# Kernel tuning notes

Hardware: AMD Instinct MI355X
Metric: run time of the kernel (lower is better)

Reference implementation:

```python
import jax, jax.numpy as jnp
import numpy as np

NUM_HEADS = 16


def setup_inputs() -> dict:
    key = jax.random.key(0)
    ks = jax.random.split(key, 6)
    B, S, E = 2, 2048, 1024
    scale = 1.0 / np.sqrt(E)
    return {
        "x": jax.random.normal(ks[0], (B, S, E), dtype=jnp.float32),
        "mask": jnp.ones((B, S), dtype=jnp.int32),
        "Wq": jax.random.normal(ks[1], (E, E), dtype=jnp.float32) * scale,
        "bq": jnp.zeros((E,), dtype=jnp.float32),
        "Wk": jax.random.normal(ks[2], (E, E), dtype=jnp.float32) * scale,
        "bk": jnp.zeros((E,), dtype=jnp.float32),
        "Wv": jax.random.normal(ks[3], (E, E), dtype=jnp.float32) * scale,
        "bv": jnp.zeros((E,), dtype=jnp.float32),
        "Wo": jax.random.normal(ks[4], (E, E), dtype=jnp.float32) * scale,
        "bo": jnp.zeros((E,), dtype=jnp.float32),
    }


def reference(x, mask, Wq, bq, Wk, bk, Wv, bv, Wo, bo):
    B, S, E = x.shape
    H = NUM_HEADS
    D = E // H

    def heads(t):  # [B,S,E] -> [B,H,S,D]
        return t.reshape(B, S, H, D).transpose(0, 2, 1, 3)

    q = heads(x @ Wq + bq)
    k = heads(x @ Wk + bk)
    v = heads(x @ Wv + bv)

    # scaled dot-product scores [B,H,S,S]
    scores = jnp.einsum("bhsd,bhtd->bhst", q, k) / jnp.sqrt(jnp.float32(D))
    m = mask.astype(jnp.float32)[:, None, None, :]  # key-side padding mask
    scores = scores + (-1e9) * (1.0 - m)
    weights = jax.nn.softmax(scores, axis=-1)
    attn = jnp.einsum("bhst,bhtd->bhsd", weights, v)

    concat = attn.transpose(0, 2, 1, 3).reshape(B, S, E)
    return concat @ Wo + bo
```

## Files before the change

kernel.cpp:

```cpp
#include <hip/hip_runtime.h>
#include <stdint.h>

#define E_DIM   1024
#define HNUM    16
#define DH      64
#define BATCH   2
#define SEQ     2048
#define M_TOT   (BATCH*SEQ)
#define LOG2E   1.44269504088896340736f

typedef __bf16 bf16x8 __attribute__((ext_vector_type(8)));
typedef __bf16 bf16x4 __attribute__((ext_vector_type(4)));
typedef float  f32x4  __attribute__((ext_vector_type(4)));
typedef float  f32x16 __attribute__((ext_vector_type(16)));
typedef unsigned short u16;
typedef unsigned int   u32;
typedef unsigned long long u64;
typedef u16 u16x8 __attribute__((ext_vector_type(8)));
typedef u32 u32x2 __attribute__((ext_vector_type(2)));
typedef u32 u32x4 __attribute__((ext_vector_type(4)));

__device__ __forceinline__ u16 f2bf(float f) {
    u32 u = __builtin_bit_cast(u32, f);
    u32 r = 0x7FFFu + ((u >> 16) & 1u);
    return (u16)((u + r) >> 16);
}

__device__ __forceinline__ void gload_lds16(const u16* g, u16* l) {
    __builtin_amdgcn_global_load_lds(
        (const __attribute__((address_space(1))) u32*)g,
        (__attribute__((address_space(3))) u32*)l, 16, 0, 0);
}

__device__ __forceinline__ u32 cvt_pk_bf16(float lo, float hi) {
    u32 r;
    asm("v_cvt_pk_bf16_f32 %0, %1, %2" : "=v"(r) : "v"(lo), "v"(hi));
    return r;
}

#define MFMA16(a,b,c) __builtin_amdgcn_mfma_f32_16x16x32_bf16((a),(b),(c),0,0,0)
#define MFMA32(a,b,c) __builtin_amdgcn_mfma_f32_32x32x16_bf16((a),(b),(c),0,0,0)

__global__ __launch_bounds__(256) void cast_x_kernel(const float* __restrict__ x,
                                                     u16* __restrict__ out, int n) {
    int idx = (blockIdx.x * 256 + threadIdx.x) * 4;
    if (idx < n) {
        float4 v = *reinterpret_cast<const float4*>(x + idx);
        ushort4 o;
        o.x = f2bf(v.x); o.y = f2bf(v.y); o.z = f2bf(v.z); o.w = f2bf(v.w);
        *reinterpret_cast<ushort4*>(out + idx) = o;
    }
}

__global__ __launch_bounds__(256) void maskbits_kernel(const int* __restrict__ mask,
                                                       u64* __restrict__ bits) {
    int i = blockIdx.x * 256 + threadIdx.x;
    u64 bl = __ballot(mask[i] != 0);
    if ((i & 63) == 0) bits[i >> 6] = bl;
}

__global__ void wtrans_kernel(const float* __restrict__ w0, const float* __restrict__ w1,
                              const float* __restrict__ w2, const float* __restrict__ w3,
                              u16* __restrict__ out) {
    __shared__ float tile[32][33];
    const float* w = blockIdx.z == 0 ? w0 : blockIdx.z == 1 ? w1 : blockIdx.z == 2 ? w2 : w3;
    const int n0 = blockIdx.x * 32, k0 = blockIdx.y * 32;
    #pragma unroll
    for (int j = 0; j < 4; j++) {
        int k = k0 + threadIdx.y + j * 8;
        tile[threadIdx.y + j * 8][threadIdx.x] = w[(size_t)k * E_DIM + n0 + threadIdx.x];
    }
    __syncthreads();
    u16* o = out + (size_t)blockIdx.z * E_DIM * E_DIM;
    #pragma unroll
    for (int j = 0; j < 4; j++) {
        int n = n0 + threadIdx.y + j * 8;
        o[(size_t)n * E_DIM + k0 + threadIdx.x] = f2bf(tile[threadIdx.x][threadIdx.y + j * 8]);
    }
}

template <typename OutT>
__global__ __launch_bounds__(256) void gemm_kernel(
    const u16* __restrict__ A, const u16* __restrict__ Bt_base, OutT* __restrict__ C_base,
    const float* __restrict__ bias0, const float* __restrict__ bias1,
    const float* __restrict__ bias2, float scale0, int Mdim) {
    const int z = blockIdx.z;
    const u16* Bt = Bt_base + (size_t)z * E_DIM * E_DIM;
    OutT* C = C_base + (size_t)z * Mdim * E_DIM;
    const float* bias = (z == 0) ? bias0 : (z == 1 ? bias1 : bias2);
    const float scale = (z == 0) ? scale0 : 1.0f;

    __shared__ __align__(16) u16 Als[128 * 32];
    __shared__ __align__(16) u16 Bls[128 * 32];

    const int tid = threadIdx.x;
    const int lane = tid & 63;
    const int w = tid >> 6;
    const int wr = (w >> 1) * 64, wc = (w & 1) * 64;
    const int tm = blockIdx.y * 128, tn = blockIdx.x * 128;
    const int r4 = tid >> 2;
    const int c8 = (tid & 3) * 8;

    f32x4 acc[4][4] = {};

    for (int k0 = 0; k0 < E_DIM; k0 += 32) {
        gload_lds16(A + (size_t)(tm + r4) * E_DIM + k0 + c8, Als + tid * 8);
        gload_lds16(A + (size_t)(tm + 64 + r4) * E_DIM + k0 + c8, Als + 2048 + tid * 8);
        gload_lds16(Bt + (size_t)(tn + r4) * E_DIM + k0 + c8, Bls + tid * 8);
        gload_lds16(Bt + (size_t)(tn + 64 + r4) * E_DIM + k0 + c8, Bls + 2048 + tid * 8);
        __syncthreads();
        const int lr = lane & 15, lg = lane >> 4;
        bf16x8 af[4], bfr[4];
        #pragma unroll
        for (int m = 0; m < 4; m++)
            af[m] = *reinterpret_cast<const bf16x8*>(Als + (wr + m * 16 + lr) * 32 + lg * 8);
        #pragma unroll
        for (int n = 0; n < 4; n++)
            bfr[n] = *reinterpret_cast<const bf16x8*>(Bls + (wc + n * 16 + lr) * 32 + lg * 8);
        #pragma unroll
        for (int m = 0; m < 4; m++)
            #pragma unroll
            for (int n = 0; n < 4; n++)
                acc[m][n] = MFMA16(af[m], bfr[n], acc[m][n]);
        __syncthreads();
    }

    const int lr = lane & 15, lg = lane >> 4;
    #pragma unroll
    for (int m = 0; m < 4; m++) {
        #pragma unroll
        for (int n = 0; n < 4; n++) {
            const int col = tn + wc + n * 16 + lr;
            const float bv = bias[col];
            #pragma unroll
            for (int r = 0; r < 4; r++) {
                const int row = tm + wr + m * 16 + lg * 4 + r;
                float v = (acc[m][n][r] + bv) * scale;
                if constexpr (sizeof(OutT) == 2) {
                    C[(size_t)row * E_DIM + col] = f2bf(v);
                } else {
                    C[(size_t)row * E_DIM + col] = v;
                }
            }
        }
    }
}

__global__ __launch_bounds__(256) void attn_kernel(
    const u16* __restrict__ Q, const u16* __restrict__ K, const u16* __restrict__ V,
    const u64* __restrict__ mbits, u16* __restrict__ PO, float* __restrict__ lws) {
    __shared__ __align__(16) u16 Kls[4][64 * 64];
    __shared__ __align__(16) u16 Vt[2][64 * 64];

    const int tid = threadIdx.x;
    const int lane = tid & 63;
    const int w = tid >> 6;
    const int hi = lane >> 5;
    const int l31 = lane & 31;
    const int n = blockIdx.x;
    const int g = n & 63, qt = n >> 6;
    const int h = g & 15, zz = g >> 4;
    const int b = zz >> 1, half = zz & 1;

    const int qrow = b * SEQ + qt * 128 + w * 32 + l31;
    bf16x8 qf[4];
    #pragma unroll
    for (int kc = 0; kc < 4; kc++)
        qf[kc] = *reinterpret_cast<const bf16x8*>(Q + (size_t)qrow * E_DIM + h * DH + kc * 16 + hi * 8);

    const int krow = (l31 & 3) | ((l31 & 4) << 1) | ((l31 & 8) >> 1) | (l31 & 16);
    const u32 ksw = (u32)(krow & 7) << 4;
    u32 koff[4];
    #pragma unroll
    for (int kc = 0; kc < 4; kc++)
        koff[kc] = (((u32)krow * 128) + (u32)kc * 32 + (u32)hi * 16) ^ ksw;

    const int krA = tid >> 3;
    const int kcA = (tid & 7) ^ (krA & 7);
    const size_t kgoffA = (size_t)krA * E_DIM + kcA * 8;
    const size_t kgoffB = kgoffA + (size_t)32 * E_DIM;

    const int vc = tid & 7;
    const int vsg = ((tid >> 3) ^ (vc << 2)) & 31;
    const size_t vgoff = (size_t)(2 * vsg) * E_DIM + vc * 8;
    u32 vwoff[8];
    #pragma unroll
    for (int j = 0; j < 8; j++)
        vwoff[j] = (((u32)(vc * 8 + j) * 128) + (u32)vsg * 4) ^ ((u32)j << 4);
    u32 vroff[4];
    #pragma unroll
    for (int kc = 0; kc < 4; kc++)
        vroff[kc] = (((u32)l31 * 128) + (u32)(2 * kc + hi) * 16) ^ (((u32)(l31 & 7)) << 4);

    f32x16 oacc0 = {}, oacc1 = {};
    float l_run = 0.f;

    const u16* Kg = K + (size_t)(b * SEQ + half * (SEQ / 2)) * E_DIM + h * DH;
    const u16* Vg = V + (size_t)(b * SEQ + half * (SEQ / 2)) * E_DIM + h * DH;
    const size_t TSTEP = (size_t)64 * E_DIM;
    const u16* kga = Kg + kgoffA;
    const u16* kgb = Kg + kgoffB;
    const u16* vgp = Vg + vgoff;
    const int NT = SEQ / 2 / 64;

    {
        u32x4 a0 = *reinterpret_cast<const u32x4*>(vgp);
        u32x4 a1 = *reinterpret_cast<const u32x4*>(vgp + E_DIM);
        gload_lds16(kga,             &Kls[0][tid * 8]);
        gload_lds16(kgb,             &Kls[0][(tid + 256) * 8]);
        gload_lds16(kga + TSTEP,     &Kls[1][tid * 8]);
        gload_lds16(kgb + TSTEP,     &Kls[1][(tid + 256) * 8]);
        gload_lds16(kga + 2 * TSTEP, &Kls[2][tid * 8]);
        gload_lds16(kgb + 2 * TSTEP, &Kls[2][(tid + 256) * 8]);
        kga += 3 * TSTEP; kgb += 3 * TSTEP; vgp += TSTEP;
        asm volatile("s_waitcnt vmcnt(2)" ::: "memory");
        __builtin_amdgcn_sched_barrier(0);
        #pragma unroll
        for (int j = 0; j < 8; j++)
            *(u32*)((char*)Vt + vwoff[j]) = __builtin_amdgcn_perm(
                a1[j >> 1], a0[j >> 1], (j & 1) ? 0x07060302u : 0x05040100u);
        asm volatile("s_waitcnt lgkmcnt(0)" ::: "memory");
        __builtin_amdgcn_sched_barrier(0);
        __builtin_amdgcn_s_barrier();
    }

    f32x16 sc0 = {}, sc1 = {};
    {
        const char* Kb = (const char*)Kls;
        __builtin_amdgcn_s_setprio(1);
        #pragma unroll
        for (int kc = 0; kc < 4; kc++) {
            bf16x8 kf0 = *(const bf16x8*)(Kb + koff[kc]);
            bf16x8 kf1 = *(const bf16x8*)(Kb + koff[kc] + 4096);
            sc0 = MFMA32(kf0, qf[kc], sc0);
            sc1 = MFMA32(kf1, qf[kc], sc1);
        }
        __builtin_amdgcn_s_setprio(0);
    }

    for (int t = 0; t < NT; t++) {
        const bool haveV = (t + 1 < NT);
        const bool haveK = (t + 3 < NT);
        u32x4 a0, a1;
        if (haveV) {
            a0 = *reinterpret_cast<const u32x4*>(vgp);
            a1 = *reinterpret_cast<const u32x4*>(vgp + E_DIM);
        }
        if (haveK) {
            gload_lds16(kga, &Kls[(t + 3) & 3][tid * 8]);
            gload_lds16(kgb, &Kls[(t + 3) & 3][(tid + 256) * 8]);
        }

        const u64 mb = mbits[b * (SEQ / 64) + half * NT + t];
        if (mb != ~0ull) {
            #pragma unroll
            for (int r = 0; r < 16; r++) {
                const int key = (r & 3) + 4 * ((r >> 2) & 1) + 8 * hi + 16 * ((r >> 3) & 1);
                if (!((mb >> key) & 1))        sc0[r] += -1.442695e9f;
                if (!((mb >> (32 + key)) & 1)) sc1[r] += -1.442695e9f;
            }
        }
        float sum = 0.f;
        #pragma unroll
        for (int r = 0; r < 16; r++) {
            sc0[r] = __builtin_amdgcn_exp2f(sc0[r]); sum += sc0[r];
        }
        #pragma unroll
        for (int r = 0; r < 16; r++) {
            sc1[r] = __builtin_amdgcn_exp2f(sc1[r]); sum += sc1[r];
        }
        l_run += sum;

        bf16x8 pf[4];
        {
            u32x4 pw0, pw1, pw2, pw3;
            #pragma unroll
            for (int e = 0; e < 4; e++) {
                pw0[e] = cvt_pk_bf16(sc0[2 * e],     sc0[2 * e + 1]);
                pw1[e] = cvt_pk_bf16(sc0[8 + 2 * e], sc0[9 + 2 * e]);
                pw2[e] = cvt_pk_bf16(sc1[2 * e],     sc1[2 * e + 1]);
                pw3[e] = cvt_pk_bf16(sc1[8 + 2 * e], sc1[9 + 2 * e]);
            }
            pf[0] = __builtin_bit_cast(bf16x8, pw0);
            pf[1] = __builtin_bit_cast(bf16x8, pw1);
            pf[2] = __builtin_bit_cast(bf16x8, pw2);
            pf[3] = __builtin_bit_cast(bf16x8, pw3);
        }

        f32x16 sn0 = {}, sn1 = {};
        if (haveV) {
            const char* Kb = (const char*)Kls + ((t + 1) & 3) * 8192;
            __builtin_amdgcn_s_setprio(1);
            #pragma unroll
            for (int kc = 0; kc < 4; kc++) {
                bf16x8 kf0 = *(const bf16x8*)(Kb + koff[kc]);
                bf16x8 kf1 = *(const bf16x8*)(Kb + koff[kc] + 4096);
                sn0 = MFMA32(kf0, qf[kc], sn0);
                sn1 = MFMA32(kf1, qf[kc], sn1);
            }
            __builtin_amdgcn_s_setprio(0);
        }

        {
            const char* Vb = (const char*)Vt + (t & 1) * 8192;
            __builtin_amdgcn_s_setprio(1);
            #pragma unroll
            for (int kc = 0; kc < 4; kc++) {
                bf16x8 vf0 = *(const bf16x8*)(Vb + vroff[kc]);
                bf16x8 vf1 = *(const bf16x8*)(Vb + vroff[kc] + 4096);
                oacc0 = MFMA32(vf0, pf[kc], oacc0);
                oacc1 = MFMA32(vf1, pf[kc], oacc1);
            }
            __builtin_amdgcn_s_setprio(0);
        }

        asm volatile("s_waitcnt vmcnt(2)" ::: "memory");
        __builtin_amdgcn_sched_barrier(0);
        if (haveV) {
            #pragma unroll
            for (int j = 0; j < 8; j++)
                *(u32*)((char*)Vt + ((t + 1) & 1) * 8192 + vwoff[j]) = __builtin_amdgcn_perm(
                    a1[j >> 1], a0[j >> 1], (j & 1) ? 0x07060302u : 0x05040100u);
        }
        asm volatile("s_waitcnt lgkmcnt(0)" ::: "memory");
        __builtin_amdgcn_sched_barrier(0);
        __builtin_amdgcn_s_barrier();

        sc0 = sn0; sc1 = sn1;
        if (haveK) { kga += TSTEP; kgb += TSTEP; }
        if (haveV) { vgp += TSTEP; }
    }

    const float l_tot = l_run + __shfl_xor(l_run, 32);
    u16* op = PO + ((size_t)half * M_TOT + qrow) * E_DIM + h * DH;
    #pragma unroll
    for (int db = 0; db < 2; db++) {
        #pragma unroll
        for (int j = 0; j < 4; j++) {
            u32x2 pk;
            pk[0] = cvt_pk_bf16(db ? oacc1[4 * j + 0] : oacc0[4 * j + 0],
                                db ? oacc1[4 * j + 1] : oacc0[4 * j + 1]);
            pk[1] = cvt_pk_bf16(db ? oacc1[4 * j + 2] : oacc0[4 * j + 2],
                                db ? oacc1[4 * j + 3] : oacc0[4 * j + 3]);
            const int d0 = 32 * db + 8 * j + 4 * hi;
            *reinterpret_cast<u32x2*>(op + d0) = pk;
        }
    }
    if (hi == 0) lws[((size_t)half * M_TOT + qrow) * HNUM + h] = l_tot;
}

__global__ __launch_bounds__(256) void combine_kernel(const u16* __restrict__ PO,
                                                      const float* __restrict__ lws,
                                                      u16* __restrict__ ab) {
    const int i = (blockIdx.x * 256 + threadIdx.x) * 8;
    const int row = i >> 10;
    const int h = (i & 1023) >> 6;
    const float l0 = lws[(size_t)row * HNUM + h];
    const float l1 = lws[((size_t)M_TOT + row) * HNUM + h];
    const float rl = 1.0f / (l0 + l1);
    const bf16x8 a = *reinterpret_cast<const bf16x8*>(PO + i);
    const bf16x8 c = *reinterpret_cast<const bf16x8*>(PO + (size_t)M_TOT * E_DIM + i);
    u16x8 o;
    #pragma unroll
    for (int j = 0; j < 8; j++)
        o[j] = f2bf(((float)a[j] + (float)c[j]) * rl);
    *reinterpret_cast<u16x8*>(ab + i) = o;
}

extern "C" void kernel_launch(void* const* d_in, const int* in_sizes, int n_in,
                              void* d_out, int out_size, void* d_ws, size_t ws_size,
                              hipStream_t stream) {
    const float* x  = (const float*)d_in[0];
    const int* mask = (const int*)d_in[1];
    const float* Wq = (const float*)d_in[2];
    const float* bq = (const float*)d_in[3];
    const float* Wk = (const float*)d_in[4];
    const float* bk = (const float*)d_in[5];
    const float* Wv = (const float*)d_in[6];
    const float* bv = (const float*)d_in[7];
    const float* Wo = (const float*)d_in[8];
    const float* bo = (const float*)d_in[9];
    float* out = (float*)d_out;

    u16* ws  = (u16*)d_ws;
    const size_t ME = (size_t)M_TOT * E_DIM;
    u16* xb  = ws;
    u16* wt  = ws + ME;
    u16* qb  = ws + 2 * ME;
    u16* kbf = ws + 3 * ME;
    u16* vbf = ws + 4 * ME;
    u64* mbf = (u64*)(ws + 5 * ME);
    float* lws = (float*)(ws + 5 * ME + 8192);
    u16* ab  = xb;
    u16* po  = (u16*)d_out;

    cast_x_kernel<<<dim3(M_TOT * E_DIM / 1024), dim3(256), 0, stream>>>(x, xb, M_TOT * E_DIM);
    wtrans_kernel<<<dim3(E_DIM / 32, E_DIM / 32, 4), dim3(32, 8), 0, stream>>>(Wq, Wk, Wv, Wo, wt);
    maskbits_kernel<<<dim3(M_TOT / 256), dim3(256), 0, stream>>>(mask, mbf);
    gemm_kernel<u16><<<dim3(E_DIM / 128, M_TOT / 128, 3), dim3(256), 0, stream>>>(
        xb, wt, qb, bq, bk, bv, 0.125f * LOG2E, M_TOT);
    attn_kernel<<<dim3(1024), dim3(256), 0, stream>>>(qb, kbf, vbf, mbf, po, lws);
    combine_kernel<<<dim3(M_TOT * E_DIM / 2048), dim3(256), 0, stream>>>(po, lws, ab);
    gemm_kernel<float><<<dim3(E_DIM / 128, M_TOT / 128, 1), dim3(256), 0, stream>>>(
        ab, wt + (size_t)3 * E_DIM * E_DIM, out, bo, bo, bo, 1.0f, M_TOT);
}
```

Measured before the change: 133.8 us.

## Drop split-KV attention and combine kernel; normalize in-kernel with ping-pong score buffers

```diff
diff --git a/kernel.cpp b/kernel.cpp
--- a/kernel.cpp
+++ b/kernel.cpp
@@ -148,7 +148,7 @@
 
 __global__ __launch_bounds__(256) void attn_kernel(
     const u16* __restrict__ Q, const u16* __restrict__ K, const u16* __restrict__ V,
-    const u64* __restrict__ mbits, u16* __restrict__ PO, float* __restrict__ lws) {
+    const u64* __restrict__ mbits, u16* __restrict__ Out) {
     __shared__ __align__(16) u16 Kls[4][64 * 64];
     __shared__ __align__(16) u16 Vt[2][64 * 64];
 
@@ -158,9 +158,8 @@
     const int hi = lane >> 5;
     const int l31 = lane & 31;
     const int n = blockIdx.x;
-    const int g = n & 63, qt = n >> 6;
-    const int h = g & 15, zz = g >> 4;
-    const int b = zz >> 1, half = zz & 1;
+    const int g = n & 31, qt = n >> 5;
+    const int h = g & 15, b = g >> 4;
 
     const int qrow = b * SEQ + qt * 128 + w * 32 + l31;
     bf16x8 qf[4];
@@ -195,13 +194,13 @@
     f32x16 oacc0 = {}, oacc1 = {};
     float l_run = 0.f;
 
-    const u16* Kg = K + (size_t)(b * SEQ + half * (SEQ / 2)) * E_DIM + h * DH;
-    const u16* Vg = V + (size_t)(b * SEQ + half * (SEQ / 2)) * E_DIM + h * DH;
+    const u16* Kg = K + (size_t)(b * SEQ) * E_DIM + h * DH;
+    const u16* Vg = V + (size_t)(b * SEQ) * E_DIM + h * DH;
     const size_t TSTEP = (size_t)64 * E_DIM;
     const u16* kga = Kg + kgoffA;
     const u16* kgb = Kg + kgoffB;
     const u16* vgp = Vg + vgoff;
-    const int NT = SEQ / 2 / 64;
+    const int NT = SEQ / 64;
 
     {
         u32x4 a0 = *reinterpret_cast<const u32x4*>(vgp);
@@ -224,7 +223,7 @@
         __builtin_amdgcn_s_barrier();
     }
 
-    f32x16 sc0 = {}, sc1 = {};
+    f32x16 sA0 = {}, sA1 = {}, sB0 = {}, sB1 = {};
     {
         const char* Kb = (const char*)Kls;
         __builtin_amdgcn_s_setprio(1);
@@ -232,13 +231,13 @@
         for (int kc = 0; kc < 4; kc++) {
             bf16x8 kf0 = *(const bf16x8*)(Kb + koff[kc]);
             bf16x8 kf1 = *(const bf16x8*)(Kb + koff[kc] + 4096);
-            sc0 = MFMA32(kf0, qf[kc], sc0);
-            sc1 = MFMA32(kf1, qf[kc], sc1);
+            sA0 = MFMA32(kf0, qf[kc], sA0);
+            sA1 = MFMA32(kf1, qf[kc], sA1);
         }
         __builtin_amdgcn_s_setprio(0);
     }
 
-    for (int t = 0; t < NT; t++) {
+    auto tile_body = [&](f32x16& c0, f32x16& c1, f32x16& n0, f32x16& n1, int t) {
         const bool haveV = (t + 1 < NT);
         const bool haveK = (t + 3 < NT);
         u32x4 a0, a1;
@@ -251,24 +250,20 @@
             gload_lds16(kgb, &Kls[(t + 3) & 3][(tid + 256) * 8]);
         }
 
-        const u64 mb = mbits[b * (SEQ / 64) + half * NT + t];
+        const u64 mb = mbits[b * NT + t];
         if (mb != ~0ull) {
             #pragma unroll
             for (int r = 0; r < 16; r++) {
                 const int key = (r & 3) + 4 * ((r >> 2) & 1) + 8 * hi + 16 * ((r >> 3) & 1);
-                if (!((mb >> key) & 1))        sc0[r] += -1.442695e9f;
-                if (!((mb >> (32 + key)) & 1)) sc1[r] += -1.442695e9f;
+                if (!((mb >> key) & 1))        c0[r] += -1.442695e9f;
+                if (!((mb >> (32 + key)) & 1)) c1[r] += -1.442695e9f;
             }
         }
         float sum = 0.f;
         #pragma unroll
-        for (int r = 0; r < 16; r++) {
-            sc0[r] = __builtin_amdgcn_exp2f(sc0[r]); sum += sc0[r];
-        }
-        #pragma unroll
-        for (int r = 0; r < 16; r++) {
-            sc1[r] = __builtin_amdgcn_exp2f(sc1[r]); sum += sc1[r];
-        }
+        for (int r = 0; r < 16; r++) { c0[r] = __builtin_amdgcn_exp2f(c0[r]); sum += c0[r]; }
+        #pragma unroll
+        for (int r = 0; r < 16; r++) { c1[r] = __builtin_amdgcn_exp2f(c1[r]); sum += c1[r]; }
         l_run += sum;
 
         bf16x8 pf[4];
@@ -276,10 +271,10 @@
             u32x4 pw0, pw1, pw2, pw3;
             #pragma unroll
             for (int e = 0; e < 4; e++) {
-                pw0[e] = cvt_pk_bf16(sc0[2 * e],     sc0[2 * e + 1]);
-                pw1[e] = cvt_pk_bf16(sc0[8 + 2 * e], sc0[9 + 2 * e]);
-                pw2[e] = cvt_pk_bf16(sc1[2 * e],     sc1[2 * e + 1]);
-                pw3[e] = cvt_pk_bf16(sc1[8 + 2 * e], sc1[9 + 2 * e]);
+                pw0[e] = cvt_pk_bf16(c0[2 * e],     c0[2 * e + 1]);
+                pw1[e] = cvt_pk_bf16(c0[8 + 2 * e], c0[9 + 2 * e]);
+                pw2[e] = cvt_pk_bf16(c1[2 * e],     c1[2 * e + 1]);
+                pw3[e] = cvt_pk_bf16(c1[8 + 2 * e], c1[9 + 2 * e]);
             }
             pf[0] = __builtin_bit_cast(bf16x8, pw0);
             pf[1] = __builtin_bit_cast(bf16x8, pw1);
@@ -287,7 +282,8 @@
             pf[3] = __builtin_bit_cast(bf16x8, pw3);
         }
 
-        f32x16 sn0 = {}, sn1 = {};
+        n0 = f32x16{};
+        n1 = f32x16{};
         if (haveV) {
             const char* Kb = (const char*)Kls + ((t + 1) & 3) * 8192;
             __builtin_amdgcn_s_setprio(1);
@@ -295,8 +291,8 @@
             for (int kc = 0; kc < 4; kc++) {
                 bf16x8 kf0 = *(const bf16x8*)(Kb + koff[kc]);
                 bf16x8 kf1 = *(const bf16x8*)(Kb + koff[kc] + 4096);
-                sn0 = MFMA32(kf0, qf[kc], sn0);
-                sn1 = MFMA32(kf1, qf[kc], sn1);
+                n0 = MFMA32(kf0, qf[kc], n0);
+                n1 = MFMA32(kf1, qf[kc], n1);
             }
             __builtin_amdgcn_s_setprio(0);
         }
@@ -326,45 +322,31 @@
         __builtin_amdgcn_sched_barrier(0);
         __builtin_amdgcn_s_barrier();
 
-        sc0 = sn0; sc1 = sn1;
         if (haveK) { kga += TSTEP; kgb += TSTEP; }
         if (haveV) { vgp += TSTEP; }
+    };
+
+    for (int tp = 0; tp < NT / 2; tp++) {
+        tile_body(sA0, sA1, sB0, sB1, 2 * tp);
+        tile_body(sB0, sB1, sA0, sA1, 2 * tp + 1);
     }
 
     const float l_tot = l_run + __shfl_xor(l_run, 32);
-    u16* op = PO + ((size_t)half * M_TOT + qrow) * E_DIM + h * DH;
+    const float rl = 1.0f / l_tot;
+    u16* op = Out + (size_t)qrow * E_DIM + h * DH;
     #pragma unroll
     for (int db = 0; db < 2; db++) {
         #pragma unroll
         for (int j = 0; j < 4; j++) {
             u32x2 pk;
-            pk[0] = cvt_pk_bf16(db ? oacc1[4 * j + 0] : oacc0[4 * j + 0],
-                                db ? oacc1[4 * j + 1] : oacc0[4 * j + 1]);
-            pk[1] = cvt_pk_bf16(db ? oacc1[4 * j + 2] : oacc0[4 * j + 2],
-                                db ? oacc1[4 * j + 3] : oacc0[4 * j + 3]);
+            pk[0] = cvt_pk_bf16((db ? oacc1[4 * j + 0] : oacc0[4 * j + 0]) * rl,
+                                (db ? oacc1[4 * j + 1] : oacc0[4 * j + 1]) * rl);
+            pk[1] = cvt_pk_bf16((db ? oacc1[4 * j + 2] : oacc0[4 * j + 2]) * rl,
+                                (db ? oacc1[4 * j + 3] : oacc0[4 * j + 3]) * rl);
             const int d0 = 32 * db + 8 * j + 4 * hi;
             *reinterpret_cast<u32x2*>(op + d0) = pk;
         }
     }
-    if (hi == 0) lws[((size_t)half * M_TOT + qrow) * HNUM + h] = l_tot;
-}
-
-__global__ __launch_bounds__(256) void combine_kernel(const u16* __restrict__ PO,
-                                                      const float* __restrict__ lws,
-                                                      u16* __restrict__ ab) {
-    const int i = (blockIdx.x * 256 + threadIdx.x) * 8;
-    const int row = i >> 10;
-    const int h = (i & 1023) >> 6;
-    const float l0 = lws[(size_t)row * HNUM + h];
-    const float l1 = lws[((size_t)M_TOT + row) * HNUM + h];
-    const float rl = 1.0f / (l0 + l1);
-    const bf16x8 a = *reinterpret_cast<const bf16x8*>(PO + i);
-    const bf16x8 c = *reinterpret_cast<const bf16x8*>(PO + (size_t)M_TOT * E_DIM + i);
-    u16x8 o;
-    #pragma unroll
-    for (int j = 0; j < 8; j++)
-        o[j] = f2bf(((float)a[j] + (float)c[j]) * rl);
-    *reinterpret_cast<u16x8*>(ab + i) = o;
 }
 
 extern "C" void kernel_launch(void* const* d_in, const int* in_sizes, int n_in,
@@ -390,17 +372,14 @@
     u16* kbf = ws + 3 * ME;
     u16* vbf = ws + 4 * ME;
     u64* mbf = (u64*)(ws + 5 * ME);
-    float* lws = (float*)(ws + 5 * ME + 8192);
     u16* ab  = xb;
-    u16* po  = (u16*)d_out;
 
     cast_x_kernel<<<dim3(M_TOT * E_DIM / 1024), dim3(256), 0, stream>>>(x, xb, M_TOT * E_DIM);
     wtrans_kernel<<<dim3(E_DIM / 32, E_DIM / 32, 4), dim3(32, 8), 0, stream>>>(Wq, Wk, Wv, Wo, wt);
     maskbits_kernel<<<dim3(M_TOT / 256), dim3(256), 0, stream>>>(mask, mbf);
     gemm_kernel<u16><<<dim3(E_DIM / 128, M_TOT / 128, 3), dim3(256), 0, stream>>>(
         xb, wt, qb, bq, bk, bv, 0.125f * LOG2E, M_TOT);
-    attn_kernel<<<dim3(1024), dim3(256), 0, stream>>>(qb, kbf, vbf, mbf, po, lws);
-    combine_kernel<<<dim3(M_TOT * E_DIM / 2048), dim3(256), 0, stream>>>(po, lws, ab);
+    attn_kernel<<<dim3(512), dim3(256), 0, stream>>>(qb, kbf, vbf, mbf, ab);
     gemm_kernel<float><<<dim3(E_DIM / 128, M_TOT / 128, 1), dim3(256), 0, stream>>>(
         ab, wt + (size_t)3 * E_DIM * E_DIM, out, bo, bo, bo, 1.0f, M_TOT);
 }
```

New measurement: 144.6 us. 1.08x slower.

## Double attention block size to 512 threads sharing K/V tiles across two query groups

Applied to the files above, without the earlier changes.

```diff
diff --git a/kernel.cpp b/kernel.cpp
--- a/kernel.cpp
+++ b/kernel.cpp
@@ -146,7 +146,7 @@
     }
 }
 
-__global__ __launch_bounds__(256) void attn_kernel(
+__global__ __launch_bounds__(512) void attn_kernel(
     const u16* __restrict__ Q, const u16* __restrict__ K, const u16* __restrict__ V,
     const u64* __restrict__ mbits, u16* __restrict__ PO, float* __restrict__ lws) {
     __shared__ __align__(16) u16 Kls[4][64 * 64];
@@ -154,7 +154,9 @@
 
     const int tid = threadIdx.x;
     const int lane = tid & 63;
-    const int w = tid >> 6;
+    const int wave = tid >> 6;
+    const int sub = wave >> 2;
+    const int wg = wave & 3;
     const int hi = lane >> 5;
     const int l31 = lane & 31;
     const int n = blockIdx.x;
@@ -162,7 +164,7 @@
     const int h = g & 15, zz = g >> 4;
     const int b = zz >> 1, half = zz & 1;
 
-    const int qrow = b * SEQ + qt * 128 + w * 32 + l31;
+    const int qrow = b * SEQ + qt * 256 + sub * 128 + wg * 32 + l31;
     bf16x8 qf[4];
     #pragma unroll
     for (int kc = 0; kc < 4; kc++)
@@ -177,16 +179,19 @@
 
     const int krA = tid >> 3;
     const int kcA = (tid & 7) ^ (krA & 7);
-    const size_t kgoffA = (size_t)krA * E_DIM + kcA * 8;
-    const size_t kgoffB = kgoffA + (size_t)32 * E_DIM;
-
-    const int vc = tid & 7;
-    const int vsg = ((tid >> 3) ^ (vc << 2)) & 31;
-    const size_t vgoff = (size_t)(2 * vsg) * E_DIM + vc * 8;
-    u32 vwoff[8];
-    #pragma unroll
-    for (int j = 0; j < 8; j++)
-        vwoff[j] = (((u32)(vc * 8 + j) * 128) + (u32)vsg * 4) ^ ((u32)j << 4);
+    const size_t kgoff = (size_t)krA * E_DIM + kcA * 8;
+
+    const int t8 = tid & 255;
+    const int vhalf = tid >> 8;
+    const int vc = t8 & 7;
+    const int vsg = ((t8 >> 3) ^ (vc << 2)) & 31;
+    const size_t vgoff = (size_t)(2 * vsg) * E_DIM + vc * 8 + vhalf * 4;
+    u32 vwoff[4];
+    #pragma unroll
+    for (int jj = 0; jj < 4; jj++) {
+        const int j = vhalf * 4 + jj;
+        vwoff[jj] = (((u32)(vc * 8 + j) * 128) + (u32)vsg * 4) ^ ((u32)j << 4);
+    }
     u32 vroff[4];
     #pragma unroll
     for (int kc = 0; kc < 4; kc++)
@@ -198,27 +203,23 @@
     const u16* Kg = K + (size_t)(b * SEQ + half * (SEQ / 2)) * E_DIM + h * DH;
     const u16* Vg = V + (size_t)(b * SEQ + half * (SEQ / 2)) * E_DIM + h * DH;
     const size_t TSTEP = (size_t)64 * E_DIM;
-    const u16* kga = Kg + kgoffA;
-    const u16* kgb = Kg + kgoffB;
+    const u16* kgp = Kg + kgoff;
     const u16* vgp = Vg + vgoff;
     const int NT = SEQ / 2 / 64;
 
     {
-        u32x4 a0 = *reinterpret_cast<const u32x4*>(vgp);
-        u32x4 a1 = *reinterpret_cast<const u32x4*>(vgp + E_DIM);
-        gload_lds16(kga,             &Kls[0][tid * 8]);
-        gload_lds16(kgb,             &Kls[0][(tid + 256) * 8]);
-        gload_lds16(kga + TSTEP,     &Kls[1][tid * 8]);
-        gload_lds16(kgb + TSTEP,     &Kls[1][(tid + 256) * 8]);
-        gload_lds16(kga + 2 * TSTEP, &Kls[2][tid * 8]);
-        gload_lds16(kgb + 2 * TSTEP, &Kls[2][(tid + 256) * 8]);
-        kga += 3 * TSTEP; kgb += 3 * TSTEP; vgp += TSTEP;
-        asm volatile("s_waitcnt vmcnt(2)" ::: "memory");
+        u32x2 a0 = *reinterpret_cast<const u32x2*>(vgp);
+        u32x2 a1 = *reinterpret_cast<const u32x2*>(vgp + E_DIM);
+        gload_lds16(kgp,             &Kls[0][tid * 8]);
+        gload_lds16(kgp + TSTEP,     &Kls[1][tid * 8]);
+        gload_lds16(kgp + 2 * TSTEP, &Kls[2][tid * 8]);
+        kgp += 3 * TSTEP; vgp += TSTEP;
+        asm volatile("s_waitcnt vmcnt(1)" ::: "memory");
         __builtin_amdgcn_sched_barrier(0);
         #pragma unroll
-        for (int j = 0; j < 8; j++)
-            *(u32*)((char*)Vt + vwoff[j]) = __builtin_amdgcn_perm(
-                a1[j >> 1], a0[j >> 1], (j & 1) ? 0x07060302u : 0x05040100u);
+        for (int jj = 0; jj < 4; jj++)
+            *(u32*)((char*)Vt + vwoff[jj]) = __builtin_amdgcn_perm(
+                a1[jj >> 1], a0[jj >> 1], (jj & 1) ? 0x07060302u : 0x05040100u);
         asm volatile("s_waitcnt lgkmcnt(0)" ::: "memory");
         __builtin_amdgcn_sched_barrier(0);
         __builtin_amdgcn_s_barrier();
@@ -241,14 +242,13 @@
     for (int t = 0; t < NT; t++) {
         const bool haveV = (t + 1 < NT);
         const bool haveK = (t + 3 < NT);
-        u32x4 a0, a1;
+        u32x2 a0, a1;
         if (haveV) {
-            a0 = *reinterpret_cast<const u32x4*>(vgp);
-            a1 = *reinterpret_cast<const u32x4*>(vgp + E_DIM);
+            a0 = *reinterpret_cast<const u32x2*>(vgp);
+            a1 = *reinterpret_cast<const u32x2*>(vgp + E_DIM);
         }
         if (haveK) {
-            gload_lds16(kga, &Kls[(t + 3) & 3][tid * 8]);
-            gload_lds16(kgb, &Kls[(t + 3) & 3][(tid + 256) * 8]);
+            gload_lds16(kgp, &Kls[(t + 3) & 3][tid * 8]);
         }
 
         const u64 mb = mbits[b * (SEQ / 64) + half * NT + t];
@@ -314,20 +314,20 @@
             __builtin_amdgcn_s_setprio(0);
         }
 
-        asm volatile("s_waitcnt vmcnt(2)" ::: "memory");
+        asm volatile("s_waitcnt vmcnt(1)" ::: "memory");
         __builtin_amdgcn_sched_barrier(0);
         if (haveV) {
             #pragma unroll
-            for (int j = 0; j < 8; j++)
-                *(u32*)((char*)Vt + ((t + 1) & 1) * 8192 + vwoff[j]) = __builtin_amdgcn_perm(
-                    a1[j >> 1], a0[j >> 1], (j & 1) ? 0x07060302u : 0x05040100u);
+            for (int jj = 0; jj < 4; jj++)
+                *(u32*)((char*)Vt + ((t + 1) & 1) * 8192 + vwoff[jj]) = __builtin_amdgcn_perm(
+                    a1[jj >> 1], a0[jj >> 1], (jj & 1) ? 0x07060302u : 0x05040100u);
         }
         asm volatile("s_waitcnt lgkmcnt(0)" ::: "memory");
         __builtin_amdgcn_sched_barrier(0);
         __builtin_amdgcn_s_barrier();
 
         sc0 = sn0; sc1 = sn1;
-        if (haveK) { kga += TSTEP; kgb += TSTEP; }
+        if (haveK) { kgp += TSTEP; }
         if (haveV) { vgp += TSTEP; }
     }
 
@@ -399,7 +399,7 @@
     maskbits_kernel<<<dim3(M_TOT / 256), dim3(256), 0, stream>>>(mask, mbf);
     gemm_kernel<u16><<<dim3(E_DIM / 128, M_TOT / 128, 3), dim3(256), 0, stream>>>(
         xb, wt, qb, bq, bk, bv, 0.125f * LOG2E, M_TOT);
-    attn_kernel<<<dim3(1024), dim3(256), 0, stream>>>(qb, kbf, vbf, mbf, po, lws);
+    attn_kernel<<<dim3(512), dim3(512), 0, stream>>>(qb, kbf, vbf, mbf, po, lws);
     combine_kernel<<<dim3(M_TOT * E_DIM / 2048), dim3(256), 0, stream>>>(po, lws, ab);
     gemm_kernel<float><<<dim3(E_DIM / 128, M_TOT / 128, 1), dim3(256), 0, stream>>>(
         ab, wt + (size_t)3 * E_DIM * E_DIM, out, bo, bo, bo, 1.0f, M_TOT);
```

Measured after the change: 128.8 us. 1.04x faster.
